# Performance work log

Measured on AMD Instinct MI355X. Metric: run time of the kernel, lower is better.

The kernel has to match this reference:

```python
import jax, jax.numpy as jnp
import numpy as np

EPS = 1e-5            # BatchNorm3d eps (running_mean=0, running_var=1 at init)
SCALE = 0.025         # patchmatch_interval_scale
NEIGHBORS = 9         # evaluate_neighbors
PROP_OUT = 1          # propagation_out_range - 1


def conv1x1(x, w):
    # 1x1x1 Conv3d, no bias: x [B,C,D,H,W], w [O,C]
    return jnp.einsum('bcdhw,oc->bodhw', x, w)


def conv_bn_relu(x, w, g, b):
    # ConvBnReLU3D with BN at init stats (mean 0, var 1)
    y = conv1x1(x, w)
    y = g[None, :, None, None, None] * y / jnp.sqrt(1.0 + EPS) + b[None, :, None, None, None]
    return jax.nn.relu(y)


def neighbor_gather_sum(x, offset):
    # x [B,D,H,W]; offset [B,2*NEIGHBORS,H,W]
    # Reflection-pad then take 9 statically-offset windows at two dilations,
    # weight each by per-pixel offsets, and average the two scales.
    B, D, H, W = x.shape
    side = int(np.sqrt(NEIGHBORS))                 # 3
    p1 = side // 2 + PROP_OUT                      # 2
    p2 = p1 * 2                                    # 4
    X1 = jnp.pad(x, ((0, 0), (0, 0), (p1, p1), (p1, p1)), mode='reflect')
    X2 = jnp.pad(x, ((0, 0), (0, 0), (p2, p2), (p2, p2)), mode='reflect')
    acc = jnp.zeros_like(x)
    for s in range(NEIGHBORS):
        iy = (s // side) * (PROP_OUT + 1)
        ix = (s % side) * (PROP_OUT + 1)
        f1 = offset[:, s, None] * X2[:, :, 2 * iy:2 * iy + H, 2 * ix:2 * ix + W]
        f = offset[:, s + NEIGHBORS, None] * X1[:, :, iy:iy + H, ix:ix + W]
        acc = acc + (f + f1) * 0.5
    return acc


def setup_inputs():
    key = jax.random.key(0)
    ks = jax.random.split(key, 10)
    B, G, D, H, W = 2, 8, 16, 256, 320
    x1 = jax.random.normal(ks[0], (B, G, D, H, W), jnp.float32)
    offset = jax.random.uniform(ks[1], (B, 2 * NEIGHBORS, H, W), jnp.float32)
    depth_min = jnp.full((B,), 425.0, jnp.float32)
    depth_max = jnp.full((B,), 935.0, jnp.float32)
    depth_sample = 425.0 + 510.0 * jax.random.uniform(ks[2], (B, D, H, W), jnp.float32)
    w = lambda k, s: 0.1 * jax.random.normal(k, s, jnp.float32)
    return dict(
        x1=x1, offset=offset, depth_sample=depth_sample,
        depth_min=depth_min, depth_max=depth_max,
        s_w0=w(ks[3], (16, G)), s_g0=jnp.ones((16,)), s_b0=jnp.zeros((16,)),
        s_w1=w(ks[4], (8, 16)), s_g1=jnp.ones((8,)), s_b1=jnp.zeros((8,)),
        s_w2=w(ks[5], (1, 8)), s_bias2=jnp.zeros((1,)),
        p_w0=w(ks[6], (16, G)), p_g0=jnp.ones((16,)), p_b0=jnp.zeros((16,)),
        p_w1=w(ks[7], (8, 16)), p_g1=jnp.ones((8,)), p_b1=jnp.zeros((8,)),
        p_w2=w(ks[8], (1, 8)), p_bias2=jnp.zeros((1,)),
    )


def reference(x1, offset, depth_sample, depth_min, depth_max,
              s_w0, s_g0, s_b0, s_w1, s_g1, s_b1, s_w2, s_bias2,
              p_w0, p_g0, p_b0, p_w1, p_g1, p_b1, p_w2, p_bias2):
    # --- PixelwiseNet: per-pixel view weight from the group cost volume ---
    h = conv_bn_relu(x1, p_w0, p_g0, p_b0)
    h = conv_bn_relu(h, p_w1, p_g1, p_b1)
    h = conv1x1(h, p_w2) + p_bias2[None, :, None, None, None]
    vw = jax.nn.sigmoid(h[:, 0])                   # [B,D,H,W]
    view_weight = jnp.max(vw, axis=1, keepdims=True)  # [B,1,H,W]

    # --- Depth_weight: adaptive neighbor depth-similarity weight ---
    inv_min = 1.0 / depth_min
    inv_max = 1.0 / depth_max
    xn = (1.0 / depth_sample - inv_max[:, None, None, None]) / \
         (inv_min - inv_max)[:, None, None, None]  # normalized inverse depth
    xg = neighbor_gather_sum(xn, offset)
    dw = jax.nn.sigmoid((2.0 - jnp.clip(jnp.abs(xg - xn) / SCALE, 0.0, 4.0)) * 2.0)

    # --- SimilarityNet on view-weighted cost volume ---
    x1w = x1 * view_weight[:, None]                # [B,G,D,H,W]
    s = conv_bn_relu(x1w, s_w0, s_g0, s_b0)
    s = conv_bn_relu(s, s_w1, s_g1, s_b1)
    s = (conv1x1(s, s_w2) + s_bias2[None, :, None, None, None])[:, 0]  # [B,D,H,W]
    score = neighbor_gather_sum(s, offset) * dw

    attn = jax.nn.softmax(score, axis=1)
    depth = jnp.sum(depth_sample * attn, axis=1)   # [B,H,W]
    return depth
```

## Files before the change

kernel.cpp:

```cpp
#include <hip/hip_runtime.h>
#include <math.h>

constexpr int B = 2, G = 8, D = 16, H = 256, W = 320;
constexpr int HW = H * W;
constexpr float EPS = 1e-5f;
constexpr int WSTRIDE = 320;

typedef _Float16 h2 __attribute__((ext_vector_type(2)));

#if __has_builtin(__builtin_amdgcn_fdot2)
#define FDOT2(a, b, c) __builtin_amdgcn_fdot2((a), (b), (c), false)
#else
#define FDOT2(a, b, c) fmaf((float)(a).x, (float)(b).x, fmaf((float)(a).y, (float)(b).y, (c)))
#endif

static __device__ __forceinline__ h2 cvtpk_(float a, float b) {
#if __has_builtin(__builtin_amdgcn_cvt_pkrtz)
    return __builtin_bit_cast(h2, __builtin_amdgcn_cvt_pkrtz(a, b));
#else
    h2 v; v.x = (_Float16)a; v.y = (_Float16)b; return v;
#endif
}

__device__ __forceinline__ float sigmoidf_(float x) {
    return 1.0f / (1.0f + __expf(-x));
}

__device__ __forceinline__ int reflect_(int i, int n) {
    return i < 0 ? -i : (i >= n ? 2 * n - 2 - i : i);
}

__device__ __forceinline__ void pack_net_(
    const float* __restrict__ w0, const float* __restrict__ g0, const float* __restrict__ b0,
    const float* __restrict__ w1, const float* __restrict__ g1, const float* __restrict__ b1,
    const float* __restrict__ w2, const float* __restrict__ bias2,
    float* __restrict__ o, int t, float rs)
{
    if (t < 64) {
        const int oo = t >> 2, j = t & 3;
        const float s = g0[oo] * rs;
        h2 v; v.x = (_Float16)(w0[oo * 8 + 2 * j] * s);
        v.y = (_Float16)(w0[oo * 8 + 2 * j + 1] * s);
        ((h2*)o)[t] = v;
    } else if (t < 128) {
        const int u = t - 64, oo = u >> 3, j = u & 7;
        const float s = g1[oo] * rs;
        h2 v; v.x = (_Float16)(w1[oo * 16 + 2 * j] * s);
        v.y = (_Float16)(w1[oo * 16 + 2 * j + 1] * s);
        ((h2*)o)[t] = v;
    } else if (t < 132) {
        const int u = t - 128;
        h2 v; v.x = (_Float16)w2[2 * u];
        v.y = (_Float16)w2[2 * u + 1];
        ((h2*)o)[t] = v;
    } else if (t < 148) {
        o[t] = b0[t - 132];
    } else if (t < 156) {
        o[t] = b1[t - 148];
    } else if (t == 156) {
        o[t] = bias2[0];
    }
}

__global__ __launch_bounds__(256) void k_prep(
    const float* __restrict__ sw0, const float* __restrict__ sg0, const float* __restrict__ sb0,
    const float* __restrict__ sw1, const float* __restrict__ sg1, const float* __restrict__ sb1,
    const float* __restrict__ sw2, const float* __restrict__ sbias2,
    const float* __restrict__ pw0, const float* __restrict__ pg0, const float* __restrict__ pb0,
    const float* __restrict__ pw1, const float* __restrict__ pg1, const float* __restrict__ pb1,
    const float* __restrict__ pw2, const float* __restrict__ pbias2,
    float* __restrict__ wbuf)
{
    const int t = threadIdx.x;
    const float rs = rsqrtf(1.0f + EPS);
    pack_net_(pw0, pg0, pb0, pw1, pg1, pb1, pw2, pbias2, wbuf, t, rs);
    pack_net_(sw0, sg0, sb0, sw1, sg1, sb1, sw2, sbias2, wbuf + WSTRIDE, t, rs);
}

__device__ __forceinline__ float2 mlph2_(const float* __restrict__ Wb,
                                         const h2 xa[4], const h2 xb[4])
{
    const h2* __restrict__ W0 = (const h2*)Wb;
    const h2* __restrict__ W1 = (const h2*)Wb + 64;
    const h2* __restrict__ W2 = (const h2*)Wb + 128;
    const float* __restrict__ B0 = Wb + 132;
    const float* __restrict__ B1 = Wb + 148;
    const h2 zz = {};

    h2 l1a[8], l1b[8];
    #pragma unroll
    for (int o = 0; o < 8; ++o) {
        float a0 = B0[2 * o], a1 = B0[2 * o + 1];
        float c0 = a0, c1 = a1;
        #pragma unroll
        for (int j = 0; j < 4; ++j) {
            const h2 wA = W0[(2 * o) * 4 + j];
            const h2 wB = W0[(2 * o + 1) * 4 + j];
            a0 = FDOT2(wA, xa[j], a0); c0 = FDOT2(wA, xb[j], c0);
            a1 = FDOT2(wB, xa[j], a1); c1 = FDOT2(wB, xb[j], c1);
        }
        l1a[o] = __builtin_elementwise_max(cvtpk_(a0, a1), zz);
        l1b[o] = __builtin_elementwise_max(cvtpk_(c0, c1), zz);
    }
    h2 l2a[4], l2b[4];
    #pragma unroll
    for (int o = 0; o < 4; ++o) {
        float a0 = B1[2 * o], a1 = B1[2 * o + 1];
        float c0 = a0, c1 = a1;
        #pragma unroll
        for (int j = 0; j < 8; ++j) {
            const h2 wA = W1[(2 * o) * 8 + j];
            const h2 wB = W1[(2 * o + 1) * 8 + j];
            a0 = FDOT2(wA, l1a[j], a0); c0 = FDOT2(wA, l1b[j], c0);
            a1 = FDOT2(wB, l1a[j], a1); c1 = FDOT2(wB, l1b[j], c1);
        }
        l2a[o] = __builtin_elementwise_max(cvtpk_(a0, a1), zz);
        l2b[o] = __builtin_elementwise_max(cvtpk_(c0, c1), zz);
    }
    float hA = Wb[156], hB = Wb[156];
    #pragma unroll
    for (int j = 0; j < 4; ++j) {
        const h2 w = W2[j];
        hA = FDOT2(w, l2a[j], hA);
        hB = FDOT2(w, l2b[j], hB);
    }
    return make_float2(hA, hB);
}

__global__ __launch_bounds__(512, 8) void k_fused(
    const float* __restrict__ x1,
    const float* __restrict__ depth_sample,
    const float* __restrict__ depth_min, const float* __restrict__ depth_max,
    const float* __restrict__ wP, const float* __restrict__ wS,
    float* __restrict__ s_out, float* __restrict__ xn_out)
{
    __shared__ float2 red[16][32];

    const int tid = threadIdx.x;
    const int pl = tid & 31;
    const int dt = tid >> 5;
    const int pid0 = blockIdx.x * 64 + 2 * pl;
    const int b = pid0 / HW;
    const int p0 = pid0 - b * HW;

    const float* xp = x1 + ((size_t)(b * G * D) + dt) * HW + p0;
    float2 xv[8];
    #pragma unroll
    for (int g = 0; g < 8; ++g)
        xv[g] = *reinterpret_cast<const float2*>(xp + (size_t)g * D * HW);
    h2 xa[4], xb[4];
    #pragma unroll
    for (int j = 0; j < 4; ++j) {
        xa[j] = cvtpk_(xv[2 * j].x, xv[2 * j + 1].x);
        xb[j] = cvtpk_(xv[2 * j].y, xv[2 * j + 1].y);
    }

    red[dt][pl] = mlph2_(wP, xa, xb);
    __syncthreads();

    float2 mx = red[0][pl];
    #pragma unroll
    for (int k = 1; k < 16; ++k) {
        const float2 r = red[k][pl];
        mx.x = fmaxf(mx.x, r.x);
        mx.y = fmaxf(mx.y, r.y);
    }
    const float vwa = sigmoidf_(mx.x);
    const float vwb = sigmoidf_(mx.y);

    h2 va; va.x = (_Float16)vwa; va.y = (_Float16)vwa;
    h2 vb; vb.x = (_Float16)vwb; vb.y = (_Float16)vwb;
    h2 xsa[4], xsb[4];
    #pragma unroll
    for (int j = 0; j < 4; ++j) { xsa[j] = xa[j] * va; xsb[j] = xb[j] * vb; }
    const float2 hS = mlph2_(wS, xsa, xsb);

    const size_t oidx = (size_t)(b * D + dt) * HW + p0;
    *reinterpret_cast<float2*>(s_out + oidx) = hS;

    const float inv_min = 1.0f / depth_min[b];
    const float inv_max = 1.0f / depth_max[b];
    const float rinv = 1.0f / (inv_min - inv_max);
    const float2 ds = *reinterpret_cast<const float2*>(depth_sample + oidx);
    *reinterpret_cast<float2*>(xn_out + oidx) =
        make_float2((1.0f / ds.x - inv_max) * rinv,
                    (1.0f / ds.y - inv_max) * rinv);
}

__global__ __launch_bounds__(1024, 8) void k_score_depth(
    const float* __restrict__ s_arr, const float* __restrict__ xn,
    const float* __restrict__ offset, const float* __restrict__ depth_sample,
    float* __restrict__ out)
{
    __shared__ float off_lds[18][64];
    __shared__ float redM[16][64];
    __shared__ float redS[16][64];
    __shared__ float redA[16][64];

    const int bid = blockIdx.x;
    const int wg = (bid & 7) * 320 + (bid >> 3);

    const int tid = threadIdx.x;
    const int pi = tid & 63;
    const int dt = tid >> 6;
    const int pg0_ = wg * 64;
    const int b = pg0_ / HW;
    const int pb0 = pg0_ - b * HW;
    const int p = pb0 + pi;
    const int h = p / W;
    const int w = p - h * W;

    const float* ob = offset + (size_t)b * 18 * HW + pb0;
    for (int idx = tid; idx < 18 * 64; idx += 1024) {
        const int s = idx >> 6, qq = idx & 63;
        off_lds[s][qq] = ob[(size_t)s * HW + qq];
    }
    __syncthreads();

    int a1s[9], a2s[9];
    {
        int ry1[3], ry2[3], cx1[3], cx2[3];
        #pragma unroll
        for (int i = 0; i < 3; ++i) {
            ry1[i] = reflect_(h + (i - 1) * 2, H) * W;
            ry2[i] = reflect_(h + (i - 1) * 4, H) * W;
            cx1[i] = reflect_(w + (i - 1) * 2, W);
            cx2[i] = reflect_(w + (i - 1) * 4, W);
        }
        #pragma unroll
        for (int s = 0; s < 9; ++s) {
            a1s[s] = ry1[s / 3] + cx1[s % 3];
            a2s[s] = ry2[s / 3] + cx2[s % 3];
        }
    }

    const size_t bbase = (size_t)b * D * HW;
    const float* sd = s_arr + bbase + (size_t)dt * HW;
    const float* xd = xn + bbase + (size_t)dt * HW;

    float accs = 0.0f, accx = 0.0f;
    #pragma unroll
    for (int s = 0; s < 9; ++s) {
        const float w1 = off_lds[s + 9][pi];
        const float w2 = off_lds[s][pi];
        accs += 0.5f * (w1 * sd[a1s[s]] + w2 * sd[a2s[s]]);
        accx += 0.5f * (w1 * xd[a1s[s]] + w2 * xd[a2s[s]]);
    }
    const float xc = xd[p];
    const float diff = fminf(fabsf(accx - xc) * 40.0f, 4.0f);
    const float dwv = sigmoidf_((2.0f - diff) * 2.0f);
    const float score = accs * dwv;
    const float dsv = depth_sample[bbase + (size_t)dt * HW + p];

    redM[dt][pi] = score;
    __syncthreads();
    float m = redM[0][pi];
    #pragma unroll
    for (int k = 1; k < 16; ++k) m = fmaxf(m, redM[k][pi]);

    const float e = __expf(score - m);
    redS[dt][pi] = e;
    redA[dt][pi] = dsv * e;
    __syncthreads();

    if (dt == 0) {
        float sum = 0.0f, acc = 0.0f;
        #pragma unroll
        for (int k = 0; k < 16; ++k) { sum += redS[k][pi]; acc += redA[k][pi]; }
        out[pg0_ + pi] = acc / sum;
    }
}

extern "C" void kernel_launch(void* const* d_in, const int* in_sizes, int n_in,
                              void* d_out, int out_size, void* d_ws, size_t ws_size,
                              hipStream_t stream)
{
    const float* x1           = (const float*)d_in[0];
    const float* offset       = (const float*)d_in[1];
    const float* depth_sample = (const float*)d_in[2];
    const float* depth_min    = (const float*)d_in[3];
    const float* depth_max    = (const float*)d_in[4];
    const float* s_w0 = (const float*)d_in[5];
    const float* s_g0 = (const float*)d_in[6];
    const float* s_b0 = (const float*)d_in[7];
    const float* s_w1 = (const float*)d_in[8];
    const float* s_g1 = (const float*)d_in[9];
    const float* s_b1 = (const float*)d_in[10];
    const float* s_w2 = (const float*)d_in[11];
    const float* s_bias2 = (const float*)d_in[12];
    const float* p_w0 = (const float*)d_in[13];
    const float* p_g0 = (const float*)d_in[14];
    const float* p_b0 = (const float*)d_in[15];
    const float* p_w1 = (const float*)d_in[16];
    const float* p_g1 = (const float*)d_in[17];
    const float* p_b1 = (const float*)d_in[18];
    const float* p_w2 = (const float*)d_in[19];
    const float* p_bias2 = (const float*)d_in[20];

    float* s_arr = (float*)d_ws;
    float* xn    = s_arr + (size_t)B * D * HW;
    float* wbuf  = xn + (size_t)B * D * HW;

    k_prep<<<1, 256, 0, stream>>>(
        s_w0, s_g0, s_b0, s_w1, s_g1, s_b1, s_w2, s_bias2,
        p_w0, p_g0, p_b0, p_w1, p_g1, p_b1, p_w2, p_bias2, wbuf);

    k_fused<<<(B * HW) / 64, 512, 0, stream>>>(
        x1, depth_sample, depth_min, depth_max,
        wbuf, wbuf + WSTRIDE, s_arr, xn);

    k_score_depth<<<(B * HW) / 64, 1024, 0, stream>>>(
        s_arr, xn, offset, depth_sample, (float*)d_out);
}
```

Before: 68.63 us.

## Stage neighbor rows of score and xn in LDS for gather reuse

The score/depth kernel now cooperatively loads a 5-row by 72-column reflected halo tile of both the similarity score and normalized inverse depth for all 16 depth planes into shared memory. The 18 neighbor gathers per thread then read from LDS instead of issuing scattered global loads. This replaces redundant global traffic with one coalesced-ish staging pass, at the cost of about 46 KB of extra shared memory per block, which drops the launch-bounds occupancy hint from 8 to 2. The staging loop also uses integer division and reflection per element.

```diff
diff --git a/kernel.cpp b/kernel.cpp
--- a/kernel.cpp
+++ b/kernel.cpp
@@ -187,11 +187,13 @@
                     (1.0f / ds.y - inv_max) * rinv);
 }
 
-__global__ __launch_bounds__(1024, 8) void k_score_depth(
+__global__ __launch_bounds__(1024, 2) void k_score_depth(
     const float* __restrict__ s_arr, const float* __restrict__ xn,
     const float* __restrict__ offset, const float* __restrict__ depth_sample,
     float* __restrict__ out)
 {
+    __shared__ float sS[16][5][72];
+    __shared__ float sX[16][5][72];
     __shared__ float off_lds[18][64];
     __shared__ float redM[16][64];
     __shared__ float redS[16][64];
@@ -206,51 +208,46 @@
     const int pg0_ = wg * 64;
     const int b = pg0_ / HW;
     const int pb0 = pg0_ - b * HW;
-    const int p = pb0 + pi;
-    const int h = p / W;
-    const int w = p - h * W;
+    const int h = pb0 / W;
+    const int w0 = pb0 - h * W;
+
+    const size_t bbase = (size_t)b * D * HW;
 
     const float* ob = offset + (size_t)b * 18 * HW + pb0;
     for (int idx = tid; idx < 18 * 64; idx += 1024) {
         const int s = idx >> 6, qq = idx & 63;
         off_lds[s][qq] = ob[(size_t)s * HW + qq];
     }
+
+    for (int idx = tid; idx < 16 * 5 * 72; idx += 1024) {
+        const int d = idx / 360;
+        const int rm = idx - d * 360;
+        const int r = rm / 72;
+        const int c = rm - r * 72;
+        const int gr = reflect_(h + (r - 2) * 2, H) * W;
+        const int gc = reflect_(w0 - 4 + c, W);
+        const size_t off = bbase + (size_t)d * HW + gr + gc;
+        sS[d][r][c] = s_arr[off];
+        sX[d][r][c] = xn[off];
+    }
     __syncthreads();
 
-    int a1s[9], a2s[9];
-    {
-        int ry1[3], ry2[3], cx1[3], cx2[3];
-        #pragma unroll
-        for (int i = 0; i < 3; ++i) {
-            ry1[i] = reflect_(h + (i - 1) * 2, H) * W;
-            ry2[i] = reflect_(h + (i - 1) * 4, H) * W;
-            cx1[i] = reflect_(w + (i - 1) * 2, W);
-            cx2[i] = reflect_(w + (i - 1) * 4, W);
-        }
-        #pragma unroll
-        for (int s = 0; s < 9; ++s) {
-            a1s[s] = ry1[s / 3] + cx1[s % 3];
-            a2s[s] = ry2[s / 3] + cx2[s % 3];
-        }
-    }
-
-    const size_t bbase = (size_t)b * D * HW;
-    const float* sd = s_arr + bbase + (size_t)dt * HW;
-    const float* xd = xn + bbase + (size_t)dt * HW;
-
     float accs = 0.0f, accx = 0.0f;
     #pragma unroll
     for (int s = 0; s < 9; ++s) {
+        const int sy = s / 3, sx = s % 3;
         const float w1 = off_lds[s + 9][pi];
         const float w2 = off_lds[s][pi];
-        accs += 0.5f * (w1 * sd[a1s[s]] + w2 * sd[a2s[s]]);
-        accx += 0.5f * (w1 * xd[a1s[s]] + w2 * xd[a2s[s]]);
-    }
-    const float xc = xd[p];
+        accs += 0.5f * (w1 * sS[dt][sy + 1][pi + 2 * sx + 2] +
+                        w2 * sS[dt][2 * sy][pi + 4 * sx]);
+        accx += 0.5f * (w1 * sX[dt][sy + 1][pi + 2 * sx + 2] +
+                        w2 * sX[dt][2 * sy][pi + 4 * sx]);
+    }
+    const float xc = sX[dt][2][pi + 4];
     const float diff = fminf(fabsf(accx - xc) * 40.0f, 4.0f);
     const float dwv = sigmoidf_((2.0f - diff) * 2.0f);
     const float score = accs * dwv;
-    const float dsv = depth_sample[bbase + (size_t)dt * HW + p];
+    const float dsv = depth_sample[bbase + (size_t)dt * HW + pb0 + pi];
 
     redM[dt][pi] = score;
     __syncthreads();
```

Measured after the change: 75.16 us. 9.5% more time.
